# Kernel tuning notes

Hardware: AMD Instinct MI355X
Metric: run time of the kernel (lower is better)

The kernel has to match this reference:

```python
import jax, jax.numpy as jnp
import numpy as np

N_U = 50000  # user nodes
N_I = 50000  # item nodes
E = 150000   # edges per edge type
C = 128      # channels (per-head out dim)
H = 8        # heads
L = 2        # layers


def setup_inputs() -> dict:
    key = jax.random.key(0)
    ks = iter(jax.random.split(key, 40))

    def nrm(shape, scale=0.1):
        return jax.random.normal(next(ks), shape, jnp.float32) * scale

    inp = {}
    inp["x_u"] = nrm((N_U, C), 1.0)
    inp["x_i"] = nrm((N_I, C), 1.0)
    # row 0 = src indices, row 1 = dst indices (both node sets have 50k nodes)
    inp["ei_ui"] = jax.random.randint(next(ks), (2, E), 0, N_U)
    inp["ei_iu"] = jax.random.randint(next(ks), (2, E), 0, N_I)
    for et in ("ui", "iu"):
        inp[f"Wsrc_{et}"] = nrm((L, C, H * C))
        inp[f"Wdst_{et}"] = nrm((L, C, H * C))
        inp[f"asrc_{et}"] = nrm((L, H, C))
        inp[f"adst_{et}"] = nrm((L, H, C))
        inp[f"b_{et}"] = jnp.zeros((L, C), jnp.float32)
    inp["Ru"] = nrm((L, C, C))
    inp["Ri"] = nrm((L, C, C))
    inp["gu"] = jnp.ones((L, C), jnp.float32)
    inp["bu"] = jnp.zeros((L, C), jnp.float32)
    inp["gi"] = jnp.ones((L, C), jnp.float32)
    inp["bi"] = jnp.zeros((L, C), jnp.float32)
    return inp


def _segment_softmax(logits, seg, n):
    # numerically stable softmax over edges grouped by destination node
    m = jax.ops.segment_max(logits, seg, num_segments=n)
    m = jnp.where(jnp.isfinite(m), m, 0.0)  # empty segments -> -inf guard
    e = jnp.exp(logits - m[seg])
    s = jax.ops.segment_sum(e, seg, num_segments=n)
    return e / (s[seg] + 1e-16)


def _gat(x_src, x_dst, ei, Wsrc, Wdst, a_src, a_dst, bias, n_dst):
    # PyG GATConv, bipartite, concat=False, no self loops, eval (no dropout)
    hs = (x_src @ Wsrc).reshape(-1, H, C)          # [N_src, H, C]
    hd = (x_dst @ Wdst).reshape(-1, H, C)          # [N_dst, H, C]
    al_s = jnp.einsum('nhc,hc->nh', hs, a_src)     # [N_src, H]
    al_d = jnp.einsum('nhc,hc->nh', hd, a_dst)     # [N_dst, H]
    src, dst = ei[0], ei[1]
    e = jax.nn.leaky_relu(al_s[src] + al_d[dst], negative_slope=0.2)  # [E, H]
    alpha = _segment_softmax(e, dst, n_dst)                           # [E, H]
    msg = alpha[:, :, None] * hs[src]                                 # [E, H, C]
    out = jax.ops.segment_sum(msg, dst, num_segments=n_dst)           # [N_dst, H, C]
    return out.mean(axis=1) + bias                                    # concat=False -> head mean


def _ln(x, g, b):
    m = x.mean(-1, keepdims=True)
    v = jnp.mean((x - m) ** 2, axis=-1, keepdims=True)
    return (x - m) * jax.lax.rsqrt(v + 1e-5) * g + b


def reference(x_u, x_i, ei_ui, ei_iu,
              Wsrc_ui, Wdst_ui, asrc_ui, adst_ui, b_ui,
              Wsrc_iu, Wdst_iu, asrc_iu, adst_iu, b_iu,
              Ru, Ri, gu, bu, gi, bi):
    for l in range(L):
        o_i = _gat(x_u, x_i, ei_ui, Wsrc_ui[l], Wdst_ui[l], asrc_ui[l], adst_ui[l], b_ui[l], N_I)
        o_u = _gat(x_i, x_u, ei_iu, Wsrc_iu[l], Wdst_iu[l], asrc_iu[l], adst_iu[l], b_iu[l], N_U)
        y_u = jax.nn.elu(_ln(o_u + x_u @ Ru[l], gu[l], bu[l])) + x_u
        y_i = jax.nn.elu(_ln(o_i + x_i @ Ri[l], gi[l], bi[l])) + x_i
        x_u, x_i = y_u, y_i
    return (x_u, x_i)
```

## Files before the change

kernel.cpp:

```cpp
#include <hip/hip_runtime.h>
#include <hip/hip_bf16.h>

#define NU 50000
#define NI 50000
#define NN 50000
#define NEDGE 150000
#define CC 128
#define HH 8
#define HCC 1024

__global__ void fold_kernel(const float* __restrict__ W0, const float* __restrict__ a0,
                            const float* __restrict__ W1, const float* __restrict__ a1,
                            const float* __restrict__ W2, const float* __restrict__ a2,
                            const float* __restrict__ W3, const float* __restrict__ a3,
                            float* __restrict__ v4) {
    int gid = blockIdx.x * blockDim.x + threadIdx.x;
    if (gid >= 4096) return;
    int mat = gid >> 10;
    int rem = gid & 1023;
    int cin = rem >> 3;
    int h   = rem & 7;
    const float* W = (mat == 0) ? W0 : (mat == 1) ? W1 : (mat == 2) ? W2 : W3;
    const float* a = (mat == 0) ? a0 : (mat == 1) ? a1 : (mat == 2) ? a2 : a3;
    const float* wrow = W + (size_t)cin * HCC + h * CC;
    const float* arow = a + h * CC;
    float acc = 0.f;
    #pragma unroll 8
    for (int c = 0; c < CC; ++c) acc += wrow[c] * arow[c];
    v4[gid] = acc;
}

__global__ __launch_bounds__(256) void al_kernel(const float* __restrict__ xu, const float* __restrict__ xi,
                          const float* __restrict__ v4,
                          float* __restrict__ al0, float* __restrict__ al1,
                          float* __restrict__ al2, float* __restrict__ al3) {
    __shared__ float xs[32][132];
    __shared__ float vs[1024];
    int cfg = blockIdx.y;
    const float* x = (cfg == 0 || cfg == 3) ? xu : xi;
    int n = NN;
    float* out = (cfg == 0) ? al0 : (cfg == 1) ? al1 : (cfg == 2) ? al2 : al3;
    const float* v = v4 + cfg * 1024;
    int n0 = blockIdx.x * 32;
    int tid = threadIdx.x;
    #pragma unroll
    for (int r = 0; r < 4; ++r) vs[tid + r * 256] = v[tid + r * 256];
    #pragma unroll
    for (int r = 0; r < 4; ++r) {
        int q = tid + r * 256;
        int row = q >> 5;
        int c4 = (q & 31) << 2;
        float4 f = make_float4(0.f, 0.f, 0.f, 0.f);
        if (n0 + row < n) f = *(const float4*)&x[(size_t)(n0 + row) * CC + c4];
        xs[row][c4] = f.x; xs[row][c4 + 1] = f.y; xs[row][c4 + 2] = f.z; xs[row][c4 + 3] = f.w;
    }
    __syncthreads();
    int nl = tid >> 3, h = tid & 7;
    if (n0 + nl < n) {
        float acc = 0.f;
        #pragma unroll 8
        for (int c = 0; c < CC; ++c) acc += xs[nl][c] * vs[c * 8 + h];
        out[(size_t)(n0 + nl) * 8 + h] = acc;
    }
}

__global__ void csr_hist_kernel(const int* __restrict__ ei_ui, const int* __restrict__ ei_iu,
                                int* __restrict__ cnt_ui, int* __restrict__ cnt_iu) {
    int t = blockIdx.x * 256 + threadIdx.x;
    if (t < NEDGE) {
        atomicAdd(&cnt_ui[ei_ui[NEDGE + t]], 1);
    } else if (t < 2 * NEDGE) {
        int e = t - NEDGE;
        atomicAdd(&cnt_iu[ei_iu[NEDGE + e]], 1);
    }
}

__global__ __launch_bounds__(1024) void csr_scan_kernel(
        const int* __restrict__ cnt_ui, int* __restrict__ off_ui, int* __restrict__ cur_ui,
        const int* __restrict__ cnt_iu, int* __restrict__ off_iu, int* __restrict__ cur_iu) {
    const int* cnt = blockIdx.x ? cnt_iu : cnt_ui;
    int* off = blockIdx.x ? off_iu : off_ui;
    int* cur = blockIdx.x ? cur_iu : cur_ui;
    __shared__ int tmp[1024];
    __shared__ int carry_s;
    int t = threadIdx.x;
    if (t == 0) carry_s = 0;
    __syncthreads();
    for (int base = 0; base < NN; base += 8192) {
        int carry = carry_s;
        int v[8]; int s = 0;
        int i0 = base + t * 8;
        #pragma unroll
        for (int j = 0; j < 8; ++j) { int idx = i0 + j; v[j] = (idx < NN) ? cnt[idx] : 0; s += v[j]; }
        tmp[t] = s; __syncthreads();
        int incl = s;
        for (int d = 1; d < 1024; d <<= 1) {
            int val = (t >= d) ? tmp[t - d] : 0;
            __syncthreads();
            incl += val;
            tmp[t] = incl;
            __syncthreads();
        }
        int run = carry + incl - s;
        #pragma unroll
        for (int j = 0; j < 8; ++j) {
            int idx = i0 + j;
            if (idx < NN) { off[idx] = run; cur[idx] = run; }
            run += v[j];
        }
        __syncthreads();
        if (t == 1023) carry_s = carry + incl;
        __syncthreads();
    }
    if (t == 0) off[NN] = carry_s;
}

__global__ void csr_fill_kernel(const int* __restrict__ ei_ui, const int* __restrict__ ei_iu,
                                int* __restrict__ cur_ui, int* __restrict__ cur_iu,
                                int* __restrict__ perm_ui, int* __restrict__ perm_iu) {
    int t = blockIdx.x * 256 + threadIdx.x;
    if (t < NEDGE) {
        int dst = ei_ui[NEDGE + t];
        int slot = atomicAdd(&cur_ui[dst], 1);
        perm_ui[slot] = t;
    } else if (t < 2 * NEDGE) {
        int e = t - NEDGE;
        int dst = ei_iu[NEDGE + e];
        int slot = atomicAdd(&cur_iu[dst], 1);
        perm_iu[slot] = e;
    }
}

__global__ __launch_bounds__(256) void agg_kernel(const int* __restrict__ ei,
                           const int* __restrict__ off, const int* __restrict__ perm,
                           const float* __restrict__ al_s, const float* __restrict__ al_d,
                           const float* __restrict__ x, float* __restrict__ agg) {
    int wv = (blockIdx.x * 256 + threadIdx.x) >> 6;
    int lane = threadIdx.x & 63;
    if (wv >= NN) return;
    int e0 = off[wv], e1 = off[wv + 1];
    int hl = lane & 7;
    float ald = al_d[(size_t)wv * 8 + hl];
    float s = 0.f;
    for (int q = e0; q < e1; ++q) {
        int e = perm[q];
        int src = ei[e];
        float t = al_s[(size_t)src * 8 + hl] + ald;
        t = (t > 0.f) ? t : 0.2f * t;
        s += expf(t);
    }
    float inv = 1.f / (8.f * (s + 1e-16f));
    float acc[8][2];
    #pragma unroll
    for (int h = 0; h < 8; ++h) { acc[h][0] = 0.f; acc[h][1] = 0.f; }
    int c = lane << 1;
    for (int q = e0; q < e1; ++q) {
        int e = perm[q];
        int src = ei[e];
        float t = al_s[(size_t)src * 8 + hl] + ald;
        t = (t > 0.f) ? t : 0.2f * t;
        float w = expf(t) * inv;
        float2 xv = *(const float2*)&x[(size_t)src * CC + c];
        #pragma unroll
        for (int h = 0; h < 8; ++h) {
            float wh = __shfl(w, h, 64);
            acc[h][0] += wh * xv.x;
            acc[h][1] += wh * xv.y;
        }
    }
    #pragma unroll
    for (int h = 0; h < 8; ++h) {
        *(float2*)&agg[(size_t)wv * HCC + h * CC + c] = make_float2(acc[h][0], acc[h][1]);
    }
}

__global__ __launch_bounds__(256) void proj_kernel(const float* __restrict__ agg, const float* __restrict__ W,
                            float* __restrict__ outp) {
    __shared__ float As[64][132];
    __shared__ float Bs[128][68];
    int tid = threadIdx.x;
    int m0 = blockIdx.x * 64;
    int j0 = blockIdx.y * 64;
    int tx = tid & 15, ty = tid >> 4;
    float acc[4][4];
    #pragma unroll
    for (int i = 0; i < 4; ++i)
        #pragma unroll
        for (int j = 0; j < 4; ++j) acc[i][j] = 0.f;

    for (int h = 0; h < 8; ++h) {
        __syncthreads();
        #pragma unroll
        for (int r = 0; r < 8; ++r) {
            int q = r * 256 + tid;
            int m = q >> 5;
            int k4 = (q & 31) << 2;
            float4 f = make_float4(0.f, 0.f, 0.f, 0.f);
            if (m0 + m < NN) f = *(const float4*)&agg[(size_t)(m0 + m) * HCC + h * CC + k4];
            *(float4*)&As[m][k4] = f;
        }
        #pragma unroll
        for (int r = 0; r < 8; ++r) {
            int q = r * 256 + tid;
            int k = q >> 4;
            int j4 = (q & 15) << 2;
            *(float4*)&Bs[k][j4] = *(const float4*)&W[(size_t)k * HCC + h * CC + j0 + j4];
        }
        __syncthreads();
        #pragma unroll 4
        for (int k4 = 0; k4 < 32; ++k4) {
            int kb = k4 << 2;
            float4 a0 = *(float4*)&As[(ty << 2) + 0][kb];
            float4 a1 = *(float4*)&As[(ty << 2) + 1][kb];
            float4 a2 = *(float4*)&As[(ty << 2) + 2][kb];
            float4 a3 = *(float4*)&As[(ty << 2) + 3][kb];
            float4 b0 = *(float4*)&Bs[kb + 0][tx << 2];
            float4 b1 = *(float4*)&Bs[kb + 1][tx << 2];
            float4 b2 = *(float4*)&Bs[kb + 2][tx << 2];
            float4 b3 = *(float4*)&Bs[kb + 3][tx << 2];
            acc[0][0] += a0.x*b0.x + a0.y*b1.x + a0.z*b2.x + a0.w*b3.x;
            acc[0][1] += a0.x*b0.y + a0.y*b1.y + a0.z*b2.y + a0.w*b3.y;
            acc[0][2] += a0.x*b0.z + a0.y*b1.z + a0.z*b2.z + a0.w*b3.z;
            acc[0][3] += a0.x*b0.w + a0.y*b1.w + a0.z*b2.w + a0.w*b3.w;
            acc[1][0] += a1.x*b0.x + a1.y*b1.x + a1.z*b2.x + a1.w*b3.x;
            acc[1][1] += a1.x*b0.y + a1.y*b1.y + a1.z*b2.y + a1.w*b3.y;
            acc[1][2] += a1.x*b0.z + a1.y*b1.z + a1.z*b2.z + a1.w*b3.z;
            acc[1][3] += a1.x*b0.w + a1.y*b1.w + a1.z*b2.w + a1.w*b3.w;
            acc[2][0] += a2.x*b0.x + a2.y*b1.x + a2.z*b2.x + a2.w*b3.x;
            acc[2][1] += a2.x*b0.y + a2.y*b1.y + a2.z*b2.y + a2.w*b3.y;
            acc[2][2] += a2.x*b0.z + a2.y*b1.z + a2.z*b2.z + a2.w*b3.z;
            acc[2][3] += a2.x*b0.w + a2.y*b1.w + a2.z*b2.w + a2.w*b3.w;
            acc[3][0] += a3.x*b0.x + a3.y*b1.x + a3.z*b2.x + a3.w*b3.x;
            acc[3][1] += a3.x*b0.y + a3.y*b1.y + a3.z*b2.y + a3.w*b3.y;
            acc[3][2] += a3.x*b0.z + a3.y*b1.z + a3.z*b2.z + a3.w*b3.z;
            acc[3][3] += a3.x*b0.w + a3.y*b1.w + a3.z*b2.w + a3.w*b3.w;
        }
    }
    #pragma unroll
    for (int i = 0; i < 4; ++i) {
        int m = m0 + (ty << 2) + i;
        if (m < NN) {
            float4 o = make_float4(acc[i][0], acc[i][1], acc[i][2], acc[i][3]);
            *(float4*)&outp[(size_t)m * CC + j0 + (tx << 2)] = o;
        }
    }
}

__global__ __launch_bounds__(256) void finalize_kernel(const float* __restrict__ o, const float* __restrict__ bias,
                                const float* __restrict__ x, const float* __restrict__ R,
                                const float* __restrict__ g, const float* __restrict__ bb,
                                float* __restrict__ y, int M) {
    __shared__ float Xt[128][68];
    __shared__ float Rs[128][132];
    int tid = threadIdx.x;
    int m0 = blockIdx.x * 64;
    #pragma unroll
    for (int r = 0; r < 8; ++r) {
        int q = r * 256 + tid;
        int row = q >> 5;
        int k4 = (q & 31) << 2;
        float4 f = make_float4(0.f, 0.f, 0.f, 0.f);
        if (m0 + row < M) f = *(const float4*)&x[(size_t)(m0 + row) * CC + k4];
        Xt[k4][row] = f.x; Xt[k4 + 1][row] = f.y; Xt[k4 + 2][row] = f.z; Xt[k4 + 3][row] = f.w;
    }
    #pragma unroll
    for (int r = 0; r < 16; ++r) {
        int q = r * 256 + tid;
        int kr = q >> 5;
        int c4 = (q & 31) << 2;
        *(float4*)&Rs[kr][c4] = *(const float4*)&R[(size_t)kr * CC + c4];
    }
    __syncthreads();
    int tx = tid & 15, ty = tid >> 4;
    int c0 = tx << 3;
    float t[4][8];
    #pragma unroll
    for (int i = 0; i < 4; ++i)
        #pragma unroll
        for (int j = 0; j < 8; ++j) t[i][j] = 0.f;
    #pragma unroll 2
    for (int k = 0; k < 128; ++k) {
        float4 av = *(float4*)&Xt[k][ty << 2];
        float4 r0 = *(float4*)&Rs[k][c0];
        float4 r1 = *(float4*)&Rs[k][c0 + 4];
        float a0 = av.x, a1 = av.y, a2 = av.z, a3 = av.w;
        t[0][0] += a0 * r0.x; t[0][1] += a0 * r0.y; t[0][2] += a0 * r0.z; t[0][3] += a0 * r0.w;
        t[0][4] += a0 * r1.x; t[0][5] += a0 * r1.y; t[0][6] += a0 * r1.z; t[0][7] += a0 * r1.w;
        t[1][0] += a1 * r0.x; t[1][1] += a1 * r0.y; t[1][2] += a1 * r0.z; t[1][3] += a1 * r0.w;
        t[1][4] += a1 * r1.x; t[1][5] += a1 * r1.y; t[1][6] += a1 * r1.z; t[1][7] += a1 * r1.w;
        t[2][0] += a2 * r0.x; t[2][1] += a2 * r0.y; t[2][2] += a2 * r0.z; t[2][3] += a2 * r0.w;
        t[2][4] += a2 * r1.x; t[2][5] += a2 * r1.y; t[2][6] += a2 * r1.z; t[2][7] += a2 * r1.w;
        t[3][0] += a3 * r0.x; t[3][1] += a3 * r0.y; t[3][2] += a3 * r0.z; t[3][3] += a3 * r0.w;
        t[3][4] += a3 * r1.x; t[3][5] += a3 * r1.y; t[3][6] += a3 * r1.z; t[3][7] += a3 * r1.w;
    }
    float4 g0 = *(const float4*)&g[c0];
    float4 g1 = *(const float4*)&g[c0 + 4];
    float4 b0 = *(const float4*)&bb[c0];
    float4 b1 = *(const float4*)&bb[c0 + 4];
    float4 bi0 = *(const float4*)&bias[c0];
    float4 bi1 = *(const float4*)&bias[c0 + 4];
    float gv[8] = { g0.x, g0.y, g0.z, g0.w, g1.x, g1.y, g1.z, g1.w };
    float bv[8] = { b0.x, b0.y, b0.z, b0.w, b1.x, b1.y, b1.z, b1.w };
    float biv[8] = { bi0.x, bi0.y, bi0.z, bi0.w, bi1.x, bi1.y, bi1.z, bi1.w };
    #pragma unroll
    for (int i = 0; i < 4; ++i) {
        int m = m0 + (ty << 2) + i;
        bool valid = (m < M);
        float s1 = 0.f, s2 = 0.f;
        if (valid) {
            float4 o0 = *(const float4*)&o[(size_t)m * CC + c0];
            float4 o1 = *(const float4*)&o[(size_t)m * CC + c0 + 4];
            float ov[8] = { o0.x, o0.y, o0.z, o0.w, o1.x, o1.y, o1.z, o1.w };
            #pragma unroll
            for (int j = 0; j < 8; ++j) {
                float val = t[i][j] + ov[j] + biv[j];
                t[i][j] = val;
                s1 += val;
                s2 += val * val;
            }
        }
        #pragma unroll
        for (int off = 1; off < 16; off <<= 1) {
            s1 += __shfl_xor(s1, off, 64);
            s2 += __shfl_xor(s2, off, 64);
        }
        if (valid) {
            float mean = s1 * (1.f / 128.f);
            float var = s2 * (1.f / 128.f) - mean * mean;
            float rstd = rsqrtf(var + 1e-5f);
            float res[8];
            #pragma unroll
            for (int j = 0; j < 8; ++j) {
                float nv = (t[i][j] - mean) * rstd * gv[j] + bv[j];
                float el = (nv > 0.f) ? nv : expm1f(nv);
                res[j] = el + Xt[c0 + j][(ty << 2) + i];
            }
            *(float4*)&y[(size_t)m * CC + c0]     = make_float4(res[0], res[1], res[2], res[3]);
            *(float4*)&y[(size_t)m * CC + c0 + 4] = make_float4(res[4], res[5], res[6], res[7]);
        }
    }
}

extern "C" void kernel_launch(void* const* d_in, const int* in_sizes, int n_in,
                              void* d_out, int out_size, void* d_ws, size_t ws_size,
                              hipStream_t stream) {
    const float* xu_in   = (const float*)d_in[0];
    const float* xi_in   = (const float*)d_in[1];
    const int*   ei_ui   = (const int*)d_in[2];
    const int*   ei_iu   = (const int*)d_in[3];
    const float* Wsrc_ui = (const float*)d_in[4];
    const float* Wdst_ui = (const float*)d_in[5];
    const float* asrc_ui = (const float*)d_in[6];
    const float* adst_ui = (const float*)d_in[7];
    const float* b_ui    = (const float*)d_in[8];
    const float* Wsrc_iu = (const float*)d_in[9];
    const float* Wdst_iu = (const float*)d_in[10];
    const float* asrc_iu = (const float*)d_in[11];
    const float* adst_iu = (const float*)d_in[12];
    const float* b_iu    = (const float*)d_in[13];
    const float* Ru      = (const float*)d_in[14];
    const float* Ri      = (const float*)d_in[15];
    const float* gu      = (const float*)d_in[16];
    const float* bu      = (const float*)d_in[17];
    const float* gi      = (const float*)d_in[18];
    const float* bi      = (const float*)d_in[19];
    float* out = (float*)d_out;

    float* xu1 = out;
    float* xi1 = out + 6400000;

    float* ws = (float*)d_ws;
    size_t off = 0;
    float* agg    = ws + off; off += (size_t)NN * HCC;
    float* acc_i  = ws + off; off += 6400000;
    float* acc_u  = ws + off; off += 6400000;
    float* al_s_ui = ws + off; off += 400000;
    float* al_d_ui = ws + off; off += 400000;
    float* al_s_iu = ws + off; off += 400000;
    float* al_d_iu = ws + off; off += 400000;
    float* v4     = ws + off; off += 4096;
    int* ib = (int*)(ws + off);
    size_t ioff = 0;
    int* off_ui  = ib + ioff; ioff += NN + 1;
    int* off_iu  = ib + ioff; ioff += NN + 1;
    int* cur_ui  = ib + ioff; ioff += NN;
    int* cur_iu  = ib + ioff; ioff += NN;
    int* cnt_ui  = ib + ioff; ioff += NN;
    int* cnt_iu  = ib + ioff; ioff += NN;
    int* perm_ui = ib + ioff; ioff += NEDGE;
    int* perm_iu = ib + ioff; ioff += NEDGE;

    hipMemsetAsync(cnt_ui, 0, NN * sizeof(int), stream);
    hipMemsetAsync(cnt_iu, 0, NN * sizeof(int), stream);
    const int ef_blocks = (2 * NEDGE + 255) / 256;
    csr_hist_kernel<<<ef_blocks, 256, 0, stream>>>(ei_ui, ei_iu, cnt_ui, cnt_iu);
    csr_scan_kernel<<<2, 1024, 0, stream>>>(cnt_ui, off_ui, cur_ui, cnt_iu, off_iu, cur_iu);
    csr_fill_kernel<<<ef_blocks, 256, 0, stream>>>(ei_ui, ei_iu, cur_ui, cur_iu, perm_ui, perm_iu);

    const int agg_blocks = (NN * 64 + 255) / 256;

    for (int l = 0; l < 2; ++l) {
        const float* xu = (l == 0) ? xu_in : xu1;
        const float* xi = (l == 0) ? xi_in : xi1;
        float* yu = (l == 0) ? xu1 : out;
        float* yi = (l == 0) ? xi1 : out + 6400000;

        fold_kernel<<<16, 256, 0, stream>>>(
            Wsrc_ui + (size_t)l * 131072, asrc_ui + (size_t)l * 1024,
            Wdst_ui + (size_t)l * 131072, adst_ui + (size_t)l * 1024,
            Wsrc_iu + (size_t)l * 131072, asrc_iu + (size_t)l * 1024,
            Wdst_iu + (size_t)l * 131072, adst_iu + (size_t)l * 1024, v4);

        al_kernel<<<dim3(1563, 4), 256, 0, stream>>>(xu, xi, v4,
                                                     al_s_ui, al_d_ui, al_s_iu, al_d_iu);

        agg_kernel<<<agg_blocks, 256, 0, stream>>>(ei_ui, off_ui, perm_ui,
                                                   al_s_ui, al_d_ui, xu, agg);
        proj_kernel<<<dim3(782, 2), 256, 0, stream>>>(agg, Wsrc_ui + (size_t)l * 131072, acc_i);

        agg_kernel<<<agg_blocks, 256, 0, stream>>>(ei_iu, off_iu, perm_iu,
                                                   al_s_iu, al_d_iu, xi, agg);
        proj_kernel<<<dim3(782, 2), 256, 0, stream>>>(agg, Wsrc_iu + (size_t)l * 131072, acc_u);

        finalize_kernel<<<782, 256, 0, stream>>>(acc_i, b_ui + (size_t)l * 128, xi,
                                                 Ri + (size_t)l * 16384, gi + (size_t)l * 128,
                                                 bi + (size_t)l * 128, yi, NI);
        finalize_kernel<<<782, 256, 0, stream>>>(acc_u, b_iu + (size_t)l * 128, xu,
                                                 Ru + (size_t)l * 16384, gu + (size_t)l * 128,
                                                 bu + (size_t)l * 128, yu, NU);
    }
}
```

Before: 1.893 ms.

## Replace FP32 SIMT projection GEMM with split-bf16 MFMA using pre-swizzled operands

The aggregation kernel now writes its per-head aggregates as hi/lo bf16 pairs in a tiled, transposed layout. The projection GEMM runs on bf16 MFMA instructions, using three products (hi·hi, hi·lo, lo·hi) to get close to fp32 accuracy. A new kernel splits and transposes the source weights once per layer. This replaces scalar FP32 FMAs with matrix-core throughput and halves the bytes per aggregate element. In exchange it adds a weight-prep launch, triples the MFMA count, and loses a little precision from dropping the lo·lo term.

```diff
diff --git a/kernel.cpp b/kernel.cpp
--- a/kernel.cpp
+++ b/kernel.cpp
@@ -8,6 +8,16 @@
 #define CC 128
 #define HH 8
 #define HCC 1024
+#define NGRP 3128
+
+typedef __attribute__((ext_vector_type(8))) short bf16x8;
+typedef __attribute__((ext_vector_type(4))) float f32x4;
+
+static __device__ inline ushort bf16_rn(float f) {
+    uint u = __float_as_uint(f);
+    uint r = (u + 0x7FFFu + ((u >> 16) & 1u)) >> 16;
+    return (ushort)r;
+}
 
 __global__ void fold_kernel(const float* __restrict__ W0, const float* __restrict__ a0,
                             const float* __restrict__ W1, const float* __restrict__ a1,
@@ -131,10 +141,28 @@
     }
 }
 
+__global__ void wprep_kernel(const float* __restrict__ Wui, const float* __restrict__ Wiu,
+                             ushort* __restrict__ hi_ui, ushort* __restrict__ lo_ui,
+                             ushort* __restrict__ hi_iu, ushort* __restrict__ lo_iu) {
+    int idx = blockIdx.x * 256 + threadIdx.x;
+    if (idx >= 131072) return;
+    const float* W = blockIdx.y ? Wiu : Wui;
+    ushort* ph = blockIdx.y ? hi_iu : hi_ui;
+    ushort* pl = blockIdx.y ? lo_iu : lo_ui;
+    int j = idx >> 10, k = idx & 1023;
+    int h = k >> 7, c = k & 127;
+    float v = W[(size_t)c * 1024 + h * 128 + j];
+    ushort hh = bf16_rn(v);
+    float lo = v - __uint_as_float((uint)hh << 16);
+    ph[idx] = hh;
+    pl[idx] = bf16_rn(lo);
+}
+
 __global__ __launch_bounds__(256) void agg_kernel(const int* __restrict__ ei,
                            const int* __restrict__ off, const int* __restrict__ perm,
                            const float* __restrict__ al_s, const float* __restrict__ al_d,
-                           const float* __restrict__ x, float* __restrict__ agg) {
+                           const float* __restrict__ x,
+                           ushort* __restrict__ aggT_hi, ushort* __restrict__ aggT_lo) {
     int wv = (blockIdx.x * 256 + threadIdx.x) >> 6;
     int lane = threadIdx.x & 63;
     if (wv >= NN) return;
@@ -168,80 +196,72 @@
             acc[h][1] += wh * xv.y;
         }
     }
+    int rgrp = wv >> 4, rr = wv & 15;
     #pragma unroll
     for (int h = 0; h < 8; ++h) {
-        *(float2*)&agg[(size_t)wv * HCC + h * CC + c] = make_float2(acc[h][0], acc[h][1]);
-    }
-}
-
-__global__ __launch_bounds__(256) void proj_kernel(const float* __restrict__ agg, const float* __restrict__ W,
-                            float* __restrict__ outp) {
-    __shared__ float As[64][132];
-    __shared__ float Bs[128][68];
+        float v0 = acc[h][0], v1 = acc[h][1];
+        ushort h0 = bf16_rn(v0);
+        ushort h1 = bf16_rn(v1);
+        float l0f = v0 - __uint_as_float((uint)h0 << 16);
+        float l1f = v1 - __uint_as_float((uint)h1 << 16);
+        ushort l0 = bf16_rn(l0f);
+        ushort l1 = bf16_rn(l1f);
+        size_t base = ((size_t)rgrp * 128 + h * 16 + (lane >> 2)) * 128 + rr * 8 + ((2 * lane) & 7);
+        *(uint*)&aggT_hi[base] = (uint)h0 | ((uint)h1 << 16);
+        *(uint*)&aggT_lo[base] = (uint)l0 | ((uint)l1 << 16);
+    }
+}
+
+__global__ __launch_bounds__(256) void proj_mfma_kernel(
+        const ushort* __restrict__ aggT_hi, const ushort* __restrict__ aggT_lo,
+        const ushort* __restrict__ WT_hi, const ushort* __restrict__ WT_lo,
+        float* __restrict__ outp) {
+    __shared__ __align__(16) ushort Bh[128][72];
+    __shared__ __align__(16) ushort Bl[128][72];
     int tid = threadIdx.x;
+    int w = tid >> 6, lane = tid & 63;
     int m0 = blockIdx.x * 64;
-    int j0 = blockIdx.y * 64;
-    int tx = tid & 15, ty = tid >> 4;
-    float acc[4][4];
-    #pragma unroll
-    for (int i = 0; i < 4; ++i)
-        #pragma unroll
-        for (int j = 0; j < 4; ++j) acc[i][j] = 0.f;
-
-    for (int h = 0; h < 8; ++h) {
+    int a = (m0 >> 4) + w;
+    int r = lane & 15, g = lane >> 4;
+    f32x4 acc[8];
+    #pragma unroll
+    for (int nt = 0; nt < 8; ++nt) acc[nt] = (f32x4){0.f, 0.f, 0.f, 0.f};
+
+    for (int kt = 0; kt < 16; ++kt) {
         __syncthreads();
         #pragma unroll
-        for (int r = 0; r < 8; ++r) {
-            int q = r * 256 + tid;
-            int m = q >> 5;
-            int k4 = (q & 31) << 2;
-            float4 f = make_float4(0.f, 0.f, 0.f, 0.f);
-            if (m0 + m < NN) f = *(const float4*)&agg[(size_t)(m0 + m) * HCC + h * CC + k4];
-            *(float4*)&As[m][k4] = f;
-        }
-        #pragma unroll
-        for (int r = 0; r < 8; ++r) {
-            int q = r * 256 + tid;
-            int k = q >> 4;
-            int j4 = (q & 15) << 2;
-            *(float4*)&Bs[k][j4] = *(const float4*)&W[(size_t)k * HCC + h * CC + j0 + j4];
+        for (int qq = 0; qq < 4; ++qq) {
+            int q = qq * 256 + tid;
+            int j = q >> 3, ck = (q & 7) * 8;
+            size_t gsrc = (size_t)j * 1024 + kt * 64 + ck;
+            *(uint4*)&Bh[j][ck] = *(const uint4*)&WT_hi[gsrc];
+            *(uint4*)&Bl[j][ck] = *(const uint4*)&WT_lo[gsrc];
         }
         __syncthreads();
-        #pragma unroll 4
-        for (int k4 = 0; k4 < 32; ++k4) {
-            int kb = k4 << 2;
-            float4 a0 = *(float4*)&As[(ty << 2) + 0][kb];
-            float4 a1 = *(float4*)&As[(ty << 2) + 1][kb];
-            float4 a2 = *(float4*)&As[(ty << 2) + 2][kb];
-            float4 a3 = *(float4*)&As[(ty << 2) + 3][kb];
-            float4 b0 = *(float4*)&Bs[kb + 0][tx << 2];
-            float4 b1 = *(float4*)&Bs[kb + 1][tx << 2];
-            float4 b2 = *(float4*)&Bs[kb + 2][tx << 2];
-            float4 b3 = *(float4*)&Bs[kb + 3][tx << 2];
-            acc[0][0] += a0.x*b0.x + a0.y*b1.x + a0.z*b2.x + a0.w*b3.x;
-            acc[0][1] += a0.x*b0.y + a0.y*b1.y + a0.z*b2.y + a0.w*b3.y;
-            acc[0][2] += a0.x*b0.z + a0.y*b1.z + a0.z*b2.z + a0.w*b3.z;
-            acc[0][3] += a0.x*b0.w + a0.y*b1.w + a0.z*b2.w + a0.w*b3.w;
-            acc[1][0] += a1.x*b0.x + a1.y*b1.x + a1.z*b2.x + a1.w*b3.x;
-            acc[1][1] += a1.x*b0.y + a1.y*b1.y + a1.z*b2.y + a1.w*b3.y;
-            acc[1][2] += a1.x*b0.z + a1.y*b1.z + a1.z*b2.z + a1.w*b3.z;
-            acc[1][3] += a1.x*b0.w + a1.y*b1.w + a1.z*b2.w + a1.w*b3.w;
-            acc[2][0] += a2.x*b0.x + a2.y*b1.x + a2.z*b2.x + a2.w*b3.x;
-            acc[2][1] += a2.x*b0.y + a2.y*b1.y + a2.z*b2.y + a2.w*b3.y;
-            acc[2][2] += a2.x*b0.z + a2.y*b1.z + a2.z*b2.z + a2.w*b3.z;
-            acc[2][3] += a2.x*b0.w + a2.y*b1.w + a2.z*b2.w + a2.w*b3.w;
-            acc[3][0] += a3.x*b0.x + a3.y*b1.x + a3.z*b2.x + a3.w*b3.x;
-            acc[3][1] += a3.x*b0.y + a3.y*b1.y + a3.z*b2.y + a3.w*b3.y;
-            acc[3][2] += a3.x*b0.z + a3.y*b1.z + a3.z*b2.z + a3.w*b3.z;
-            acc[3][3] += a3.x*b0.w + a3.y*b1.w + a3.z*b2.w + a3.w*b3.w;
-        }
-    }
-    #pragma unroll
-    for (int i = 0; i < 4; ++i) {
-        int m = m0 + (ty << 2) + i;
-        if (m < NN) {
-            float4 o = make_float4(acc[i][0], acc[i][1], acc[i][2], acc[i][3]);
-            *(float4*)&outp[(size_t)m * CC + j0 + (tx << 2)] = o;
+        #pragma unroll
+        for (int kk2 = 0; kk2 < 2; ++kk2) {
+            int ks = kt * 2 + kk2;
+            int kb = ks * 4 + g;
+            size_t abase = ((size_t)a * 128 + kb) * 128 + r * 8;
+            bf16x8 a_h = *(const bf16x8*)&aggT_hi[abase];
+            bf16x8 a_l = *(const bf16x8*)&aggT_lo[abase];
+            int ko = kk2 * 32 + g * 8;
+            #pragma unroll
+            for (int nt = 0; nt < 8; ++nt) {
+                bf16x8 b_h = *(const bf16x8*)&Bh[nt * 16 + r][ko];
+                bf16x8 b_l = *(const bf16x8*)&Bl[nt * 16 + r][ko];
+                acc[nt] = __builtin_amdgcn_mfma_f32_16x16x32_bf16(a_h, b_h, acc[nt], 0, 0, 0);
+                acc[nt] = __builtin_amdgcn_mfma_f32_16x16x32_bf16(a_h, b_l, acc[nt], 0, 0, 0);
+                acc[nt] = __builtin_amdgcn_mfma_f32_16x16x32_bf16(a_l, b_h, acc[nt], 0, 0, 0);
+            }
+        }
+    }
+    #pragma unroll
+    for (int nt = 0; nt < 8; ++nt) {
+        #pragma unroll
+        for (int j = 0; j < 4; ++j) {
+            int m = m0 + w * 16 + g * 4 + j;
+            if (m < NN) outp[(size_t)m * CC + nt * 16 + r] = acc[nt][j];
         }
     }
 }
@@ -371,7 +391,8 @@
 
     float* ws = (float*)d_ws;
     size_t off = 0;
-    float* agg    = ws + off; off += (size_t)NN * HCC;
+    ushort* aggT_hi = (ushort*)(ws + off); off += (size_t)NGRP * 128 * 128 / 2;
+    ushort* aggT_lo = (ushort*)(ws + off); off += (size_t)NGRP * 128 * 128 / 2;
     float* acc_i  = ws + off; off += 6400000;
     float* acc_u  = ws + off; off += 6400000;
     float* al_s_ui = ws + off; off += 400000;
@@ -379,6 +400,10 @@
     float* al_s_iu = ws + off; off += 400000;
     float* al_d_iu = ws + off; off += 400000;
     float* v4     = ws + off; off += 4096;
+    ushort* wT_hi_ui = (ushort*)(ws + off); off += 65536;
+    ushort* wT_lo_ui = (ushort*)(ws + off); off += 65536;
+    ushort* wT_hi_iu = (ushort*)(ws + off); off += 65536;
+    ushort* wT_lo_iu = (ushort*)(ws + off); off += 65536;
     int* ib = (int*)(ws + off);
     size_t ioff = 0;
     int* off_ui  = ib + ioff; ioff += NN + 1;
@@ -398,6 +423,7 @@
     csr_fill_kernel<<<ef_blocks, 256, 0, stream>>>(ei_ui, ei_iu, cur_ui, cur_iu, perm_ui, perm_iu);
 
     const int agg_blocks = (NN * 64 + 255) / 256;
+    const int proj_blocks = (NN + 63) / 64;
 
     for (int l = 0; l < 2; ++l) {
         const float* xu = (l == 0) ? xu_in : xu1;
@@ -414,13 +440,19 @@
         al_kernel<<<dim3(1563, 4), 256, 0, stream>>>(xu, xi, v4,
                                                      al_s_ui, al_d_ui, al_s_iu, al_d_iu);
 
+        wprep_kernel<<<dim3(512, 2), 256, 0, stream>>>(
+            Wsrc_ui + (size_t)l * 131072, Wsrc_iu + (size_t)l * 131072,
+            wT_hi_ui, wT_lo_ui, wT_hi_iu, wT_lo_iu);
+
         agg_kernel<<<agg_blocks, 256, 0, stream>>>(ei_ui, off_ui, perm_ui,
-                                                   al_s_ui, al_d_ui, xu, agg);
-        proj_kernel<<<dim3(782, 2), 256, 0, stream>>>(agg, Wsrc_ui + (size_t)l * 131072, acc_i);
+                                                   al_s_ui, al_d_ui, xu, aggT_hi, aggT_lo);
+        proj_mfma_kernel<<<proj_blocks, 256, 0, stream>>>(aggT_hi, aggT_lo,
+                                                          wT_hi_ui, wT_lo_ui, acc_i);
 
         agg_kernel<<<agg_blocks, 256, 0, stream>>>(ei_iu, off_iu, perm_iu,
-                                                   al_s_iu, al_d_iu, xi, agg);
-        proj_kernel<<<dim3(782, 2), 256, 0, stream>>>(agg, Wsrc_iu + (size_t)l * 131072, acc_u);
+                                                   al_s_iu, al_d_iu, xi, aggT_hi, aggT_lo);
+        proj_mfma_kernel<<<proj_blocks, 256, 0, stream>>>(aggT_hi, aggT_lo,
+                                                          wT_hi_iu, wT_lo_iu, acc_u);
 
         finalize_kernel<<<782, 256, 0, stream>>>(acc_i, b_ui + (size_t)l * 128, xi,
                                                  Ri + (size_t)l * 16384, gi + (size_t)l * 128,
```

New measurement: 1.745 ms. -7.8%, faster.
